# Performance work log

Hardware: AMD Instinct MI355X
Metric: run time of the kernel (lower is better)

The kernel has to match this reference:

```python
import jax, jax.numpy as jnp
import numpy as np

H = 256          # decoder_size
V = 3            # vocab_size
MAX_LENGTH = 64


def lstm_cell(x, h, c, Wih, Whh, b):
    # PyTorch gate order: i, f, g, o
    g = x @ Wih.T + h @ Whh.T + b
    i, f, gg, o = jnp.split(g, 4, axis=-1)
    c = jax.nn.sigmoid(f) * c + jax.nn.sigmoid(i) * jnp.tanh(gg)
    h = jax.nn.sigmoid(o) * jnp.tanh(c)
    return h, c


def setup_inputs() -> dict:
    key = jax.random.key(0)
    ks = jax.random.split(key, 16)
    T, B, F = 512, 32, 1024
    s = 1.0 / np.sqrt(H)
    u = lambda k, shape: jax.random.uniform(k, shape, jnp.float32, -s, s)
    return dict(
        cnn_feats=jax.random.normal(ks[0], (T, B, F), jnp.float32),
        # bidirectional encoder LSTM (1 layer)
        enc_Wih_f=u(ks[1], (4 * H, F)), enc_Whh_f=u(ks[2], (4 * H, H)), enc_b_f=u(ks[3], (4 * H,)),
        enc_Wih_b=u(ks[4], (4 * H, F)), enc_Whh_b=u(ks[5], (4 * H, H)), enc_b_b=u(ks[6], (4 * H,)),
        # 2-layer decoder LSTM
        dec_Wih0=u(ks[7], (4 * H, H)), dec_Whh0=u(ks[8], (4 * H, H)), dec_b0=u(ks[9], (4 * H,)),
        dec_Wih1=u(ks[10], (4 * H, H)), dec_Whh1=u(ks[11], (4 * H, H)), dec_b1=u(ks[12], (4 * H,)),
        # per-step output projection
        lin_W=u(ks[13], (V, H)), lin_b=u(ks[14], (V,)),
    )


def _forward(cnn_feats, enc_Wih_f, enc_Whh_f, enc_b_f, enc_Wih_b, enc_Whh_b, enc_b_b,
             dec_Wih0, dec_Whh0, dec_b0, dec_Wih1, dec_Whh1, dec_b1, lin_W, lin_b):
    B = cnn_feats.shape[1]
    z = jnp.zeros((B, H), cnn_feats.dtype)

    def run_dir(seq, Wih, Whh, b):
        def step(carry, x):
            h, c = lstm_cell(x, carry[0], carry[1], Wih, Whh, b)
            return (h, c), None
        (h, c), _ = jax.lax.scan(step, (z, z), seq)
        return h, c

    # encoder final states: fwd over seq, bwd over reversed seq
    hf, cf = run_dir(cnn_feats, enc_Wih_f, enc_Whh_f, enc_b_f)
    hb, cb = run_dir(cnn_feats[::-1], enc_Wih_b, enc_Whh_b, enc_b_b)

    # decoder: layer0 init = fwd-dir state, layer1 init = bwd-dir state
    def dstep(carry, _):
        x, h0, c0, h1, c1 = carry
        h0, c0 = lstm_cell(x, h0, c0, dec_Wih0, dec_Whh0, dec_b0)
        h1, c1 = lstm_cell(h0, h1, c1, dec_Wih1, dec_Whh1, dec_b1)
        y = h1 @ lin_W.T + lin_b
        return (h1, h0, c0, h1, c1), y

    _, ys = jax.lax.scan(dstep, (z, hf, cf, hb, cb), None, length=MAX_LENGTH)
    return ys  # (MAX_LENGTH, B, V)


def reference(cnn_feats, enc_Wih_f, enc_Whh_f, enc_b_f, enc_Wih_b, enc_Whh_b, enc_b_b,
              dec_Wih0, dec_Whh0, dec_b0, dec_Wih1, dec_Whh1, dec_b1, lin_W, lin_b):
    return _forward(cnn_feats, enc_Wih_f, enc_Whh_f, enc_b_f, enc_Wih_b, enc_Whh_b, enc_b_b,
                    dec_Wih0, dec_Whh0, dec_b0, dec_Wih1, dec_Whh1, dec_b1, lin_W, lin_b)
```

## Files before the change

kernel.cpp:

```cpp
#include <hip/hip_runtime.h>
#include <stdint.h>
#include <stddef.h>

typedef __attribute__((ext_vector_type(8))) short  short8;
typedef __attribute__((ext_vector_type(4))) float  floatx4;
typedef __attribute__((ext_vector_type(4))) unsigned int u32x4;
typedef unsigned long long u64;

#define SENT 0xAAAAAAAAAAAAAAAAull

static __device__ __forceinline__ float b2f(uint16_t h) {
  union { uint32_t u; float f; } v; v.u = ((uint32_t)h) << 16; return v.f;
}
static __device__ __forceinline__ uint16_t f2b(float f) {
  union { float f; uint32_t u; } v; v.f = f;
  uint32_t u = v.u;
  uint32_t r = u + 0x7FFFu + ((u >> 16) & 1u);
  return (uint16_t)(r >> 16);
}
static __device__ __forceinline__ float sigm(float x)  { return 1.0f / (1.0f + __expf(-x)); }
static __device__ __forceinline__ float tanh_f(float x){ return 1.0f - 2.0f / (1.0f + __expf(2.0f * x)); }

static __device__ __forceinline__ floatx4 mfma16(short8 a, short8 b, floatx4 c) {
  return __builtin_amdgcn_mfma_f32_16x16x32_bf16(a, b, c, 0, 0, 0);
}
static __device__ __forceinline__ short8 cvt8(const float* p) {
  short8 r;
  #pragma unroll
  for (int i = 0; i < 8; ++i) r[i] = (short)f2b(p[i]);
  return r;
}

static __device__ __forceinline__ void st_h64(uint16_t* p, u64 v) {
  __hip_atomic_store((u64*)p, v, __ATOMIC_RELAXED, __HIP_MEMORY_SCOPE_AGENT);
}
static __device__ __forceinline__ u64 ld_h64(const u64* p) {
  return __hip_atomic_load(p, __ATOMIC_RELAXED, __HIP_MEMORY_SCOPE_AGENT);
}
static __device__ __forceinline__ bool frag_ok(u32x4 v) {
  const u64 lo = ((u64)v[1] << 32) | v[0];
  const u64 hi = ((u64)v[3] << 32) | v[2];
  return (lo != SENT) & (hi != SENT);
}
static __device__ __forceinline__ void ld8x16(const uint16_t* p, u32x4* o) {
  asm volatile(
      "global_load_dwordx4 %0, %8, off sc0 sc1\n\t"
      "global_load_dwordx4 %1, %8, off offset:64 sc0 sc1\n\t"
      "global_load_dwordx4 %2, %8, off offset:128 sc0 sc1\n\t"
      "global_load_dwordx4 %3, %8, off offset:192 sc0 sc1\n\t"
      "global_load_dwordx4 %4, %8, off offset:256 sc0 sc1\n\t"
      "global_load_dwordx4 %5, %8, off offset:320 sc0 sc1\n\t"
      "global_load_dwordx4 %6, %8, off offset:384 sc0 sc1\n\t"
      "global_load_dwordx4 %7, %8, off offset:448 sc0 sc1\n\t"
      "s_waitcnt vmcnt(0)"
      : "=&v"(o[0]), "=&v"(o[1]), "=&v"(o[2]), "=&v"(o[3]),
        "=&v"(o[4]), "=&v"(o[5]), "=&v"(o[6]), "=&v"(o[7])
      : "v"(p)
      : "memory");
}
static __device__ __forceinline__ void ld16x16(const uint16_t* pa, const uint16_t* pb,
                                               u32x4* oa, u32x4* ob) {
  asm volatile(
      "global_load_dwordx4 %0, %16, off sc0 sc1\n\t"
      "global_load_dwordx4 %1, %16, off offset:64 sc0 sc1\n\t"
      "global_load_dwordx4 %2, %16, off offset:128 sc0 sc1\n\t"
      "global_load_dwordx4 %3, %16, off offset:192 sc0 sc1\n\t"
      "global_load_dwordx4 %4, %16, off offset:256 sc0 sc1\n\t"
      "global_load_dwordx4 %5, %16, off offset:320 sc0 sc1\n\t"
      "global_load_dwordx4 %6, %16, off offset:384 sc0 sc1\n\t"
      "global_load_dwordx4 %7, %16, off offset:448 sc0 sc1\n\t"
      "global_load_dwordx4 %8, %17, off sc0 sc1\n\t"
      "global_load_dwordx4 %9, %17, off offset:64 sc0 sc1\n\t"
      "global_load_dwordx4 %10, %17, off offset:128 sc0 sc1\n\t"
      "global_load_dwordx4 %11, %17, off offset:192 sc0 sc1\n\t"
      "global_load_dwordx4 %12, %17, off offset:256 sc0 sc1\n\t"
      "global_load_dwordx4 %13, %17, off offset:320 sc0 sc1\n\t"
      "global_load_dwordx4 %14, %17, off offset:384 sc0 sc1\n\t"
      "global_load_dwordx4 %15, %17, off offset:448 sc0 sc1\n\t"
      "s_waitcnt vmcnt(0)"
      : "=&v"(oa[0]), "=&v"(oa[1]), "=&v"(oa[2]), "=&v"(oa[3]),
        "=&v"(oa[4]), "=&v"(oa[5]), "=&v"(oa[6]), "=&v"(oa[7]),
        "=&v"(ob[0]), "=&v"(ob[1]), "=&v"(ob[2]), "=&v"(ob[3]),
        "=&v"(ob[4]), "=&v"(ob[5]), "=&v"(ob[6]), "=&v"(ob[7])
      : "v"(pa), "v"(pb)
      : "memory");
}
static __device__ __forceinline__ void valve8(const uint16_t* p, u32x4* o) {
  const u64* q = (const u64*)p;
  #pragma unroll
  for (int k = 0; k < 8; ++k) {
    u64 a = ld_h64(q + k * 8), c = ld_h64(q + k * 8 + 1);
    o[k][0] = (unsigned)a; o[k][1] = (unsigned)(a >> 32);
    o[k][2] = (unsigned)c; o[k][3] = (unsigned)(c >> 32);
  }
}
static __device__ __forceinline__ void poll8f(const uint16_t* p, u32x4* o) {
  int it = 0;
  for (;;) {
    if ((++it & 1023) == 0) valve8(p, o); else ld8x16(p, o);
    bool ok = true;
    #pragma unroll
    for (int k = 0; k < 8; ++k) ok &= frag_ok(o[k]);
    if (ok) break;
    __builtin_amdgcn_s_sleep(1);
  }
}
static __device__ __forceinline__ void poll16f(const uint16_t* pa, const uint16_t* pb,
                                               u32x4* oa, u32x4* ob) {
  int it = 0;
  for (;;) {
    if ((++it & 1023) == 0) { valve8(pa, oa); valve8(pb, ob); }
    else ld16x16(pa, pb, oa, ob);
    bool ok = true;
    #pragma unroll
    for (int k = 0; k < 8; ++k) ok &= frag_ok(oa[k]) & frag_ok(ob[k]);
    if (ok) break;
    __builtin_amdgcn_s_sleep(1);
  }
}

#define H 256
#define FH 1024
#define BATCH 32
#define TSEQ 512
#define DSTEPS 64
#define ERING 8

__global__ __launch_bounds__(256) void gemm_xw(
    const float* __restrict__ A, const float* __restrict__ W,
    const float* __restrict__ bias, void* __restrict__ Cout, int out_f32)
{
  const int K = 1024, N = 1024;
  __shared__ uint16_t Ah[64 * 40], Al[64 * 40];
  __shared__ uint16_t Wh[64 * 40], Wl[64 * 40];
  const int m0 = blockIdx.x * 64;
  const int n0 = blockIdx.y * 64;
  const int tid = threadIdx.x;
  const int lane = tid & 63, w = tid >> 6;
  const int wm = w & 1, wn = w >> 1;
  const int l15 = lane & 15, q4 = lane >> 4;
  const int ldrow = tid >> 2, ldk = (tid & 3) * 8;

  floatx4 acc[2][2];
  for (int i = 0; i < 2; ++i) for (int j = 0; j < 2; ++j) acc[i][j] = (floatx4){0.f,0.f,0.f,0.f};

  for (int kb = 0; kb < K; kb += 32) {
    float aa[8], ww[8];
    {
      const float4* ap = (const float4*)(A + (size_t)(m0 + ldrow) * K + kb + ldk);
      const float4* wp = (const float4*)(W + (size_t)(n0 + ldrow) * K + kb + ldk);
      *(float4*)(aa) = ap[0]; *(float4*)(aa + 4) = ap[1];
      *(float4*)(ww) = wp[0]; *(float4*)(ww + 4) = wp[1];
    }
    short8 ah, al, wh, wl;
    #pragma unroll
    for (int i = 0; i < 8; ++i) {
      uint16_t h = f2b(aa[i]); ah[i] = (short)h; al[i] = (short)f2b(aa[i] - b2f(h));
      uint16_t g = f2b(ww[i]); wh[i] = (short)g; wl[i] = (short)f2b(ww[i] - b2f(g));
    }
    __syncthreads();
    *(short8*)(Ah + ldrow * 40 + ldk) = ah;
    *(short8*)(Al + ldrow * 40 + ldk) = al;
    *(short8*)(Wh + ldrow * 40 + ldk) = wh;
    *(short8*)(Wl + ldrow * 40 + ldk) = wl;
    __syncthreads();
    short8 afh[2], afl[2], bfh[2], bfl[2];
    #pragma unroll
    for (int mt = 0; mt < 2; ++mt) {
      afh[mt] = *(const short8*)(Ah + (wm * 32 + mt * 16 + l15) * 40 + q4 * 8);
      afl[mt] = *(const short8*)(Al + (wm * 32 + mt * 16 + l15) * 40 + q4 * 8);
    }
    #pragma unroll
    for (int nt = 0; nt < 2; ++nt) {
      bfh[nt] = *(const short8*)(Wh + (wn * 32 + nt * 16 + l15) * 40 + q4 * 8);
      bfl[nt] = *(const short8*)(Wl + (wn * 32 + nt * 16 + l15) * 40 + q4 * 8);
    }
    #pragma unroll
    for (int mt = 0; mt < 2; ++mt)
      #pragma unroll
      for (int nt = 0; nt < 2; ++nt) {
        acc[mt][nt] = mfma16(afh[mt], bfh[nt], acc[mt][nt]);
        acc[mt][nt] = mfma16(afh[mt], bfl[nt], acc[mt][nt]);
        acc[mt][nt] = mfma16(afl[mt], bfh[nt], acc[mt][nt]);
      }
  }
  #pragma unroll
  for (int mt = 0; mt < 2; ++mt)
    #pragma unroll
    for (int nt = 0; nt < 2; ++nt) {
      const int col = n0 + wn * 32 + nt * 16 + l15;
      const float bv = bias[col];
      #pragma unroll
      for (int r = 0; r < 4; ++r) {
        const int row = m0 + wm * 32 + mt * 16 + q4 * 4 + r;
        const float v = acc[mt][nt][r] + bv;
        if (out_f32) ((float*)Cout)[(size_t)row * N + col] = v;
        else         ((uint16_t*)Cout)[(size_t)row * N + col] = f2b(v);
      }
    }
}

__global__ __launch_bounds__(256, 1) void enc_fused(
    const float* __restrict__ cnn,
    const float* __restrict__ WihF, const float* __restrict__ bF,
    const float* __restrict__ WihB, const float* __restrict__ bB,
    const void* __restrict__ XgF, const void* __restrict__ XgB, int xg_f32,
    const float* __restrict__ WhhF, const float* __restrict__ WhhB,
    uint16_t* __restrict__ hslots,
    uint16_t* __restrict__ hfin, float* __restrict__ cfin,
    unsigned int* __restrict__ xgflags)
{
  if (blockIdx.x >= 16) {
    const int K = 1024, N = 1024;
    __shared__ uint16_t Ah[64 * 40], Al[64 * 40];
    __shared__ uint16_t Wh[64 * 40], Wl[64 * 40];
    const int bx = (int)blockIdx.x - 16;
    const int kk = bx >> 5, sub = bx & 31;
    const int dirg = sub >> 4, nb = sub & 15;
    const int mb = dirg ? (255 - kk) : kk;
    const float* A    = cnn;
    const float* W    = dirg ? WihB : WihF;
    const float* bias = dirg ? bB : bF;
    uint32_t* Co = (uint32_t*)(dirg ? XgB : XgF);
    const int m0 = mb * 64, n0 = nb * 64;
    const int tid = threadIdx.x;
    const int lane = tid & 63, w = tid >> 6;
    const int wm = w & 1, wn = w >> 1;
    const int l15 = lane & 15, q4 = lane >> 4;
    const int ldrow = tid >> 2, ldk = (tid & 3) * 8;

    floatx4 acc[2][2];
    for (int i = 0; i < 2; ++i) for (int j = 0; j < 2; ++j) acc[i][j] = (floatx4){0.f,0.f,0.f,0.f};

    for (int kb = 0; kb < K; kb += 32) {
      float aa[8], ww[8];
      {
        const float4* ap = (const float4*)(A + (size_t)(m0 + ldrow) * K + kb + ldk);
        const float4* wp = (const float4*)(W + (size_t)(n0 + ldrow) * K + kb + ldk);
        *(float4*)(aa) = ap[0]; *(float4*)(aa + 4) = ap[1];
        *(float4*)(ww) = wp[0]; *(float4*)(ww + 4) = wp[1];
      }
      short8 ah, al, wh, wl;
      #pragma unroll
      for (int i = 0; i < 8; ++i) {
        uint16_t h = f2b(aa[i]); ah[i] = (short)h; al[i] = (short)f2b(aa[i] - b2f(h));
        uint16_t g = f2b(ww[i]); wh[i] = (short)g; wl[i] = (short)f2b(ww[i] - b2f(g));
      }
      __syncthreads();
      *(short8*)(Ah + ldrow * 40 + ldk) = ah;
      *(short8*)(Al + ldrow * 40 + ldk) = al;
      *(short8*)(Wh + ldrow * 40 + ldk) = wh;
      *(short8*)(Wl + ldrow * 40 + ldk) = wl;
      __syncthreads();
      short8 afh[2], afl[2], bfh[2], bfl[2];
      #pragma unroll
      for (int mt = 0; mt < 2; ++mt) {
        afh[mt] = *(const short8*)(Ah + (wm * 32 + mt * 16 + l15) * 40 + q4 * 8);
        afl[mt] = *(const short8*)(Al + (wm * 32 + mt * 16 + l15) * 40 + q4 * 8);
      }
      #pragma unroll
      for (int nt = 0; nt < 2; ++nt) {
        bfh[nt] = *(const short8*)(Wh + (wn * 32 + nt * 16 + l15) * 40 + q4 * 8);
        bfl[nt] = *(const short8*)(Wl + (wn * 32 + nt * 16 + l15) * 40 + q4 * 8);
      }
      #pragma unroll
      for (int mt = 0; mt < 2; ++mt)
        #pragma unroll
        for (int nt = 0; nt < 2; ++nt) {
          acc[mt][nt] = mfma16(afh[mt], bfh[nt], acc[mt][nt]);
          acc[mt][nt] = mfma16(afh[mt], bfl[nt], acc[mt][nt]);
          acc[mt][nt] = mfma16(afl[mt], bfh[nt], acc[mt][nt]);
        }
    }
    #pragma unroll
    for (int mt = 0; mt < 2; ++mt)
      #pragma unroll
      for (int nt = 0; nt < 2; ++nt) {
        const int col = n0 + wn * 32 + nt * 16 + l15;
        const float bv = bias[col];
        #pragma unroll
        for (int r = 0; r < 4; ++r) {
          const int row = m0 + wm * 32 + mt * 16 + q4 * 4 + r;
          union { float f; uint32_t u; } cv; cv.f = acc[mt][nt][r] + bv;
          __hip_atomic_store(Co + (size_t)row * N + col, cv.u,
                             __ATOMIC_RELAXED, __HIP_MEMORY_SCOPE_AGENT);
        }
      }
    __syncthreads();
    if (threadIdx.x == 0)
      __hip_atomic_fetch_add(&xgflags[dirg * 256 + mb], 1u,
                             __ATOMIC_RELEASE, __HIP_MEMORY_SCOPE_AGENT);
    return;
  }

  const int d = blockIdx.x >> 3, q = blockIdx.x & 7;
  const void*  Xg  = d ? XgB : XgF;
  const float* Whh = d ? WhhB : WhhF;
  uint16_t* hsl = hslots + d * (ERING * BATCH * H);
  const int jOff = q * 32;
  const int tid = threadIdx.x, lane = tid & 63, w = tid >> 6;
  const int tt = w & 1, nt = w >> 1, l15 = lane & 15, q4 = lane >> 4;
  const int b = nt * 16 + l15;
  const int jg = jOff + tt * 16 + q4 * 4;

  short8 Af[4][8];
  #pragma unroll
  for (int g = 0; g < 4; ++g) {
    const int grow = g * H + jOff + tt * 16 + l15;
    #pragma unroll
    for (int ks = 0; ks < 8; ++ks)
      Af[g][ks] = cvt8(Whh + (size_t)grow * H + ks * 32 + q4 * 8);
  }

  float cc[4] = {0.f, 0.f, 0.f, 0.f};
  union HV { uint16_t u16[4]; u64 v; } hv; hv.v = 0ull;

  int mb_prev = -1;
  auto waitflag = [&](int s2) {
    const int t2 = d ? (TSEQ - 1 - s2) : s2;
    const int mb = t2 >> 1;
    if (mb != mb_prev) {
      const unsigned int* fp = xgflags + d * 256 + mb;
      while (__hip_atomic_load(fp, __ATOMIC_ACQUIRE, __HIP_MEMORY_SCOPE_AGENT) < 16u)
        __builtin_amdgcn_s_sleep(8);
      mb_prev = mb;
    }
  };

  float xvf[16];
  u64   xvb[4];
  auto ldx = [&](int s2) {
    const int t2 = d ? (TSEQ - 1 - s2) : s2;
    const size_t bas = (size_t)(t2 * BATCH + b) * FH + jg;
    if (xg_f32) {
      const float* xp = (const float*)Xg + bas;
      *(float4*)(xvf + 0)  = *(const float4*)(xp);
      *(float4*)(xvf + 4)  = *(const float4*)(xp + H);
      *(float4*)(xvf + 8)  = *(const float4*)(xp + 2 * H);
      *(float4*)(xvf + 12) = *(const float4*)(xp + 3 * H);
    } else {
      const uint16_t* xp = (const uint16_t*)Xg + bas;
      xvb[0] = *(const u64*)(xp);
      xvb[1] = *(const u64*)(xp + H);
      xvb[2] = *(const u64*)(xp + 2 * H);
      xvb[3] = *(const u64*)(xp + 3 * H);
    }
  };
  waitflag(0);
  ldx(0);

  for (int s = 0; s < TSEQ; ++s) {
    floatx4 a0 = {0.f,0.f,0.f,0.f}, a1 = a0, a2 = a0, a3 = a0;
    if (s > 0) {
      u32x4 pol[8];
      const uint16_t* ps = hsl + ((s - 1) & (ERING - 1)) * (BATCH * H) + b * H + q4 * 8;
      poll8f(ps, pol);
      #pragma unroll
      for (int ks = 0; ks < 8; ++ks) {
        short8 bfv = *(short8*)&pol[ks];
        a0 = mfma16(Af[0][ks], bfv, a0);
        a1 = mfma16(Af[1][ks], bfv, a1);
        a2 = mfma16(Af[2][ks], bfv, a2);
        a3 = mfma16(Af[3][ks], bfv, a3);
      }
    }
    #pragma unroll
    for (int r = 0; r < 4; ++r) {
      const float x0 = xg_f32 ? xvf[0 + r]  : b2f((uint16_t)(xvb[0] >> (16 * r)));
      const float x1 = xg_f32 ? xvf[4 + r]  : b2f((uint16_t)(xvb[1] >> (16 * r)));
      const float x2 = xg_f32 ? xvf[8 + r]  : b2f((uint16_t)(xvb[2] >> (16 * r)));
      const float x3 = xg_f32 ? xvf[12 + r] : b2f((uint16_t)(xvb[3] >> (16 * r)));
      const float gi = a0[r] + x0;
      const float gf = a1[r] + x1;
      const float gc = a2[r] + x2;
      const float go = a3[r] + x3;
      const float cn2 = sigm(gf) * cc[r] + sigm(gi) * tanh_f(gc);
      cc[r] = cn2;
      hv.u16[r] = f2b(sigm(go) * tanh_f(cn2));
    }
    st_h64(hsl + (s & (ERING - 1)) * (BATCH * H) + b * H + jg, hv.v);
    if (s >= 6)
      st_h64(hsl + ((s - 6) & (ERING - 1)) * (BATCH * H) + b * H + jg, SENT);
    if (s + 1 < TSEQ) { waitflag(s + 1); ldx(s + 1); }
  }
  #pragma unroll
  for (int r = 0; r < 4; ++r) {
    hfin[d * (BATCH * H) + b * H + jg + r] = hv.u16[r];
    cfin[d * (BATCH * H) + b * H + jg + r] = cc[r];
  }
}

__global__ __launch_bounds__(256, 1) void dec_rnn(
    const float* __restrict__ Wih0, const float* __restrict__ Whh0, const float* __restrict__ bb0,
    const float* __restrict__ Wih1, const float* __restrict__ Whh1, const float* __restrict__ bb1,
    const uint16_t* __restrict__ hfin, const float* __restrict__ cfin,
    uint16_t* __restrict__ h0slots,
    uint16_t* __restrict__ h1slots,
    float*    __restrict__ h1f)
{
  const int L = blockIdx.x >> 3, q = blockIdx.x & 7;
  const float* Wih = L ? Wih1 : Wih0;
  const float* Whh = L ? Whh1 : Whh0;
  const float* bs  = L ? bb1 : bb0;
  const int jOff = q * 32;
  const int tid = threadIdx.x, lane = tid & 63, w = tid >> 6;
  const int tt = w & 1, nt = w >> 1, l15 = lane & 15, q4 = lane >> 4;
  const int b = nt * 16 + l15;
  const int jg = jOff + tt * 16 + q4 * 4;

  short8 Af[4][16];
  #pragma unroll
  for (int g = 0; g < 4; ++g) {
    const int grow = g * H + jOff + tt * 16 + l15;
    #pragma unroll
    for (int ks = 0; ks < 8; ++ks) {
      Af[g][ks]     = cvt8(Wih + (size_t)grow * H + ks * 32 + q4 * 8);
      Af[g][8 + ks] = cvt8(Whh + (size_t)grow * H + ks * 32 + q4 * 8);
    }
  }
  float brg[4][4];
  #pragma unroll
  for (int g = 0; g < 4; ++g)
    #pragma unroll
    for (int r = 0; r < 4; ++r)
      brg[g][r] = bs[g * H + jOff + tt * 16 + q4 * 4 + r];

  float cc[4];
  #pragma unroll
  for (int r = 0; r < 4; ++r) cc[r] = cfin[L * (BATCH * H) + b * H + jg + r];

  uint16_t*       hOwn = L ? h1slots : h0slots;
  const uint16_t* hX   = L ? h0slots : h1slots;
  const int fo = b * H + q4 * 8;
  union HV { uint16_t u16[4]; u64 v; } hv; hv.v = 0ull;

  for (int t = 0; t < DSTEPS; ++t) {
    u32x4 pol[16];
    if (t == 0) {
      const uint16_t* ph = hfin + L * (BATCH * H) + fo;
      #pragma unroll
      for (int k = 0; k < 8; ++k) pol[8 + k] = *(const u32x4*)(ph + k * 32);
      if (L == 0) {
        #pragma unroll
        for (int k = 0; k < 8; ++k) pol[k] = (u32x4){0u, 0u, 0u, 0u};
      } else {
        poll8f(hX + fo, pol);
      }
    } else {
      const uint16_t* pOwn = hOwn + (size_t)(t - 1) * (BATCH * H) + fo;
      const uint16_t* pX   = L ? (hX + (size_t)t * (BATCH * H) + fo)
                               : (hX + (size_t)(t - 1) * (BATCH * H) + fo);
      poll16f(pX, pOwn, pol, pol + 8);
    }

    floatx4 a0 = {0.f,0.f,0.f,0.f}, a1 = a0, a2 = a0, a3 = a0;
    #pragma unroll
    for (int ks = 0; ks < 16; ++ks) {
      short8 bfv = *(short8*)&pol[ks];
      a0 = mfma16(Af[0][ks], bfv, a0);
      a1 = mfma16(Af[1][ks], bfv, a1);
      a2 = mfma16(Af[2][ks], bfv, a2);
      a3 = mfma16(Af[3][ks], bfv, a3);
    }
    float hval[4];
    #pragma unroll
    for (int r = 0; r < 4; ++r) {
      const float gi = a0[r] + brg[0][r];
      const float gf = a1[r] + brg[1][r];
      const float gc = a2[r] + brg[2][r];
      const float go = a3[r] + brg[3][r];
      const float cn2 = sigm(gf) * cc[r] + sigm(gi) * tanh_f(gc);
      cc[r] = cn2;
      hval[r] = sigm(go) * tanh_f(cn2);
      hv.u16[r] = f2b(hval[r]);
    }
    st_h64(hOwn + (size_t)t * (BATCH * H) + b * H + jg, hv.v);
    if (L == 1) {
      float* df = h1f + (size_t)t * (BATCH * H) + b * H + jg;
      #pragma unroll
      for (int r = 0; r < 4; ++r) df[r] = hval[r];
    }
  }
}

__global__ __launch_bounds__(256) void out_proj(
    const float* __restrict__ h1f, const float* __restrict__ linW,
    const float* __restrict__ linb, float* __restrict__ out)
{
  const int idx = blockIdx.x * 256 + threadIdx.x;
  if (idx >= DSTEPS * BATCH * 3) return;
  const int v = idx % 3;
  const int tb = idx / 3;
  const float* hrow = h1f + (size_t)tb * H;
  const float* wrow = linW + (size_t)v * H;
  float s = linb[v];
  for (int k = 0; k < H; ++k) s += hrow[k] * wrow[k];
  out[idx] = s;
}

extern "C" void kernel_launch(void* const* d_in, const int* in_sizes, int n_in,
                              void* d_out, int out_size, void* d_ws, size_t ws_size,
                              hipStream_t stream) {
  (void)in_sizes; (void)n_in; (void)out_size;
  const float* cnn   = (const float*)d_in[0];
  const float* WihF  = (const float*)d_in[1];
  const float* WhhF  = (const float*)d_in[2];
  const float* bF    = (const float*)d_in[3];
  const float* WihB  = (const float*)d_in[4];
  const float* WhhB  = (const float*)d_in[5];
  const float* bB    = (const float*)d_in[6];
  const float* Wih0  = (const float*)d_in[7];
  const float* Whh0  = (const float*)d_in[8];
  const float* b0    = (const float*)d_in[9];
  const float* Wih1  = (const float*)d_in[10];
  const float* Whh1  = (const float*)d_in[11];
  const float* b1    = (const float*)d_in[12];
  const float* linW  = (const float*)d_in[13];
  const float* linb  = (const float*)d_in[14];

  const size_t XG_ELEMS = (size_t)TSEQ * BATCH * FH;
  const size_t SMALL = 2459648;
  const int xg_f32 = (ws_size >= 2 * XG_ELEMS * 4 + SMALL) ? 1 : 0;
  const size_t S = XG_ELEMS * (xg_f32 ? 4 : 2);

  uint8_t* ws = (uint8_t*)d_ws;
  void*     XgF    = (void*)(ws);
  void*     XgB    = (void*)(ws + S);
  float*    h1f    = (float*)(ws + S);
  uint8_t*  base   = ws + 2 * S;
  uint16_t* hslotsE = (uint16_t*)(base);
  uint16_t* h0slots = (uint16_t*)(base + 262144);
  uint16_t* h1slots = (uint16_t*)(base + 1310720);
  uint16_t* hfin    = (uint16_t*)(base + 2359296);
  float*    cfin    = (float*)(base + 2392064);
  unsigned int* xgflags = (unsigned int*)(base + 2457600);

  hipMemsetAsync(base, 0xAA, 2359296, stream);

  if (xg_f32) {
    hipMemsetAsync(base + 2457600, 0x00, 2048, stream);
    enc_fused<<<16 + 8192, 256, 0, stream>>>(
        cnn, WihF, bF, WihB, bB, XgF, XgB, 1, WhhF, WhhB,
        hslotsE, hfin, cfin, xgflags);
  } else {
    hipMemsetAsync(base + 2457600, 0xFF, 2048, stream);
    gemm_xw<<<dim3(256, 16), 256, 0, stream>>>(cnn, WihF, bF, XgF, 0);
    gemm_xw<<<dim3(256, 16), 256, 0, stream>>>(cnn, WihB, bB, XgB, 0);
    enc_fused<<<16, 256, 0, stream>>>(
        cnn, WihF, bF, WihB, bB, XgF, XgB, 0, WhhF, WhhB,
        hslotsE, hfin, cfin, xgflags);
  }
  dec_rnn<<<16, 256, 0, stream>>>(Wih0, Whh0, b0, Wih1, Whh1, b1,
                                  hfin, cfin, h0slots, h1slots, h1f);
  out_proj<<<24, 256, 0, stream>>>(h1f, linW, linb, (float*)d_out);
}
```

Before: 2.345 ms.

## Batch-check 16 producer flags per poll and pad LDS to isolate recurrent blocks

The encoder recurrence now reads 16 consecutive input-projection completion flags with four vector loads. When all of them are set, it marks the whole range done so it can skip per-step flag polling, and otherwise it falls back to spinning on the single needed flag. A 64KB shared-memory pad, touched only under an impossible argument value, is added to the fused kernel to raise LDS usage. The apparent intent is to limit how many GEMM blocks co-reside with the latency-critical recurrent blocks on a CU. The pad reduces occupancy for the GEMM producer blocks, which can slow the input projection, and the batched check adds extra loads when flags are not yet ready.

```diff
diff --git a/kernel.cpp b/kernel.cpp
--- a/kernel.cpp
+++ b/kernel.cpp
@@ -85,6 +85,17 @@
       : "v"(pa), "v"(pb)
       : "memory");
 }
+static __device__ __forceinline__ void ld4x16f(const unsigned int* p, u32x4* o) {
+  asm volatile(
+      "global_load_dwordx4 %0, %4, off sc0 sc1\n\t"
+      "global_load_dwordx4 %1, %4, off offset:16 sc0 sc1\n\t"
+      "global_load_dwordx4 %2, %4, off offset:32 sc0 sc1\n\t"
+      "global_load_dwordx4 %3, %4, off offset:48 sc0 sc1\n\t"
+      "s_waitcnt vmcnt(0)"
+      : "=&v"(o[0]), "=&v"(o[1]), "=&v"(o[2]), "=&v"(o[3])
+      : "v"(p)
+      : "memory");
+}
 static __device__ __forceinline__ void valve8(const uint16_t* p, u32x4* o) {
   const u64* q = (const u64*)p;
   #pragma unroll
@@ -210,6 +221,9 @@
     uint16_t* __restrict__ hfin, float* __restrict__ cfin,
     unsigned int* __restrict__ xgflags)
 {
+  __shared__ uint8_t ldspad[65536];
+  if (xg_f32 == 31415) ((volatile uint8_t*)ldspad)[threadIdx.x] = 1;
+
   if (blockIdx.x >= 16) {
     const int K = 1024, N = 1024;
     __shared__ uint16_t Ah[64 * 40], Al[64 * 40];
@@ -315,16 +329,27 @@
   float cc[4] = {0.f, 0.f, 0.f, 0.f};
   union HV { uint16_t u16[4]; u64 v; } hv; hv.v = 0ull;
 
-  int mb_prev = -1;
-  auto waitflag = [&](int s2) {
-    const int t2 = d ? (TSEQ - 1 - s2) : s2;
-    const int mb = t2 >> 1;
-    if (mb != mb_prev) {
-      const unsigned int* fp = xgflags + d * 256 + mb;
-      while (__hip_atomic_load(fp, __ATOMIC_ACQUIRE, __HIP_MEMORY_SCOPE_AGENT) < 16u)
-        __builtin_amdgcn_s_sleep(8);
-      mb_prev = mb;
-    }
+  int done = -1;
+  auto waitidx = [&](int k) {
+    if (k <= done) return;
+    const int bi = k < 240 ? k : 240;
+    const unsigned int* fb = xgflags + d * 256 + (d ? (240 - bi) : bi);
+    u32x4 fv[4];
+    ld4x16f(fb, fv);
+    bool all = true;
+    #pragma unroll
+    for (int i = 0; i < 4; ++i)
+      #pragma unroll
+      for (int j = 0; j < 4; ++j) all &= (fv[i][j] >= 16u);
+    if (all) {
+      __builtin_amdgcn_fence(__ATOMIC_ACQUIRE, "agent");
+      done = bi + 15;
+      return;
+    }
+    const unsigned int* fk = xgflags + d * 256 + (d ? (255 - k) : k);
+    while (__hip_atomic_load(fk, __ATOMIC_ACQUIRE, __HIP_MEMORY_SCOPE_AGENT) < 16u)
+      __builtin_amdgcn_s_sleep(8);
+    done = k;
   };
 
   float xvf[16];
@@ -346,7 +371,7 @@
       xvb[3] = *(const u64*)(xp + 3 * H);
     }
   };
-  waitflag(0);
+  waitidx(0);
   ldx(0);
 
   for (int s = 0; s < TSEQ; ++s) {
@@ -381,7 +406,7 @@
     st_h64(hsl + (s & (ERING - 1)) * (BATCH * H) + b * H + jg, hv.v);
     if (s >= 6)
       st_h64(hsl + ((s - 6) & (ERING - 1)) * (BATCH * H) + b * H + jg, SENT);
-    if (s + 1 < TSEQ) { waitflag(s + 1); ldx(s + 1); }
+    if (s + 1 < TSEQ) { waitidx((s + 1) >> 1); ldx(s + 1); }
   }
   #pragma unroll
   for (int r = 0; r < 4; ++r) {
```

New measurement: 2.314 ms. No clear change (-1.3%).
